# Performance work log

Measured on AMD Instinct MI355X. Metric: run time of the kernel, lower is better.

The kernel has to match this reference:

```python
import jax, jax.numpy as jnp
import numpy as np

N_USERS = 50000
N_ENTITIES = 100000
CHANNEL = 64
N_FACTORS = 4
N_REL = 9  # n_relations; weight has N_REL-1 rows
N_EDGES = 1_500_000
NNZ = 800_000
N_HOPS = 2


def _l2_normalize(x, eps=1e-12):
    # matches torch F.normalize(dim=1)
    n = jnp.sqrt(jnp.sum(x * x, axis=1, keepdims=True))
    return x / jnp.maximum(n, eps)


def _distance_correlation(t1, t2):
    # t1, t2: [d] rows of disen_weight_att (d = n_relations-1)
    ch = t1.shape[0]
    t1 = t1[:, None]
    t2 = t2[:, None]
    a_ = (t1 @ t1.T) * 2.0
    b_ = (t2 @ t2.T) * 2.0
    t1s = t1 ** 2
    t2s = t2 ** 2
    a = jnp.sqrt(jnp.maximum(t1s - a_ + t1s.T, 0.0) + 1e-8)
    b = jnp.sqrt(jnp.maximum(t2s - b_ + t2s.T, 0.0) + 1e-8)
    A = a - a.mean(axis=0, keepdims=True) - a.mean(axis=1, keepdims=True) + a.mean()
    B = b - b.mean(axis=0, keepdims=True) - b.mean(axis=1, keepdims=True) + b.mean()
    dcov_AB = jnp.sqrt(jnp.maximum((A * B).sum() / ch ** 2, 0.0) + 1e-8)
    dcov_AA = jnp.sqrt(jnp.maximum((A * A).sum() / ch ** 2, 0.0) + 1e-8)
    dcov_BB = jnp.sqrt(jnp.maximum((B * B).sum() / ch ** 2, 0.0) + 1e-8)
    return dcov_AB / jnp.sqrt(dcov_AA * dcov_BB + 1e-8)


def _cul_cor(disen_weight_att):
    cor = jnp.asarray(0.0, disen_weight_att.dtype)
    for i in range(N_FACTORS):
        for j in range(i + 1, N_FACTORS):
            cor = cor + _distance_correlation(disen_weight_att[i], disen_weight_att[j])
    return cor


def setup_inputs() -> dict:
    key = jax.random.key(0)
    ks = jax.random.split(key, 11)
    return {
        "user_emb": jax.random.normal(ks[0], (N_USERS, CHANNEL), jnp.float32) * 0.1,
        "entity_emb": jax.random.normal(ks[1], (N_ENTITIES, CHANNEL), jnp.float32) * 0.1,
        "latent_emb": jax.random.normal(ks[2], (N_FACTORS, CHANNEL), jnp.float32) * 0.1,
        "weight": jax.random.normal(ks[3], (N_REL - 1, CHANNEL), jnp.float32) * 0.1,
        "disen_weight_att": jax.random.normal(ks[4], (N_FACTORS, N_REL - 1), jnp.float32) * 0.1,
        "interact_vals": jax.random.uniform(ks[5], (NNZ,), jnp.float32),
        "head": jax.random.randint(ks[6], (N_EDGES,), 0, N_ENTITIES),
        "tail": jax.random.randint(ks[7], (N_EDGES,), 0, N_ENTITIES),
        "edge_type": jax.random.randint(ks[8], (N_EDGES,), 1, N_REL),  # in [1, N_REL-1]
        "interact_rows": jax.random.randint(ks[9], (NNZ,), 0, N_USERS),
        "interact_cols": jax.random.randint(ks[10], (NNZ,), 0, N_ENTITIES),
    }


def reference(user_emb, entity_emb, latent_emb, weight, disen_weight_att,
              interact_vals, head, tail, edge_type, interact_rows, interact_cols):
    n_entities = entity_emb.shape[0]
    n_users = user_emb.shape[0]
    cor = _cul_cor(disen_weight_att)

    entity_res = entity_emb
    user_res = user_emb
    ones_e = jnp.ones((head.shape[0],), entity_emb.dtype)
    cnt = jax.ops.segment_sum(ones_e, head, num_segments=n_entities)  # reused: head fixed
    cnt = jnp.maximum(cnt, 1.0)[:, None]

    for _ in range(N_HOPS):
        # KG aggregate: gather tail emb * relation emb, scatter-mean by head
        rel_emb = weight[edge_type - 1]                      # [E, C]
        msg = entity_emb[tail] * rel_emb                     # [E, C]
        entity_agg = jax.ops.segment_sum(msg, head, num_segments=n_entities) / cnt

        # user -> latent factor attention
        score = jax.nn.softmax(user_emb @ latent_emb.T, axis=1)   # [U, F]

        # user aggregate: sparse.mm(interact_mat, entity_emb)
        gathered = interact_vals[:, None] * entity_emb[interact_cols]  # [nnz, C]
        user_agg = jax.ops.segment_sum(gathered, interact_rows, num_segments=n_users)

        disen_weight = jax.nn.softmax(disen_weight_att, axis=-1) @ weight  # [F, C]
        mix = score @ disen_weight                                          # [U, C]
        user_new = user_agg * mix + user_agg

        entity_emb = _l2_normalize(entity_agg)
        user_emb = _l2_normalize(user_new)
        entity_res = entity_res + entity_emb
        user_res = user_res + user_emb

    return entity_res, user_res, cor
```

## Files before the change

### kernel.cpp

```cpp
#include <hip/hip_runtime.h>
#include <math.h>

constexpr int CH         = 64;
constexpr int N_USERS    = 50000;
constexpr int N_ENTITIES = 100000;
constexpr int N_FACTORS  = 4;
constexpr int N_RELM1    = 8;
constexpr int N_EDGES    = 1500000;
constexpr int NNZ        = 800000;

constexpr int NBE        = (N_ENTITIES + 255) / 256;
constexpr int NBU        = (N_USERS + 255) / 256;
constexpr int NBKT       = NBE + NBU;
constexpr int TOTAL      = N_EDGES + NNZ;
constexpr int IPB        = 4096;
constexpr int NBLK       = (TOTAL + IPB - 1) / IPB;
constexpr int CAP_E      = 4352;
constexpr int CAP_U      = 4608;
constexpr int ENT_BLK8   = N_ENTITIES / 8;
constexpr int USR_BLK8   = N_USERS / 8;

typedef unsigned int u32;
typedef float __attribute__((ext_vector_type(4))) f32x4;

__device__ __forceinline__ u32 pack_bf16x2(float a, float b) {
    u32 ua = __float_as_uint(a), ub = __float_as_uint(b);
    u32 ra = (ua + 0x7FFFu + ((ua >> 16) & 1u)) >> 16;
    u32 rb = (ub + 0x7FFFu + ((ub >> 16) & 1u)) >> 16;
    return ra | (rb << 16);
}
__device__ __forceinline__ float bf_lo(u32 v) { return __uint_as_float(v << 16); }
__device__ __forceinline__ float bf_hi(u32 v) { return __uint_as_float(v & 0xFFFF0000u); }

__device__ __forceinline__ float4 nt_ld4f(const float4* p) {
    f32x4 v = __builtin_nontemporal_load((const f32x4*)p);
    return make_float4(v.x, v.y, v.z, v.w);
}
__device__ __forceinline__ void nt_st4f(float4* p, float4 v) {
    f32x4 t; t.x = v.x; t.y = v.y; t.z = v.z; t.w = v.w;
    __builtin_nontemporal_store(t, (f32x4*)p);
}
__device__ __forceinline__ int   nt_ldi(const int* p)   { return __builtin_nontemporal_load(p); }
__device__ __forceinline__ float nt_ldf(const float* p) { return __builtin_nontemporal_load(p); }

__device__ __forceinline__ uint4 gz(const u32* __restrict__ t, int r, int c8, bool v) {
    uint4 x = make_uint4(0u, 0u, 0u, 0u);
    if (v) x = ((const uint4*)t)[r * 8 + c8];
    return x;
}


__global__ __launch_bounds__(256)
void fused_stage(const int* __restrict__ head, const int* __restrict__ tail,
                 const int* __restrict__ etype,
                 const int* __restrict__ irows, const int* __restrict__ icols,
                 const float* __restrict__ ivals,
                 int* __restrict__ Bcnt,
                 u32* __restrict__ stageE, u32* __restrict__ stageU,
                 float* __restrict__ stageUv) {
    __shared__ int hist[NBKT];
    __shared__ int cur[NBKT];
    for (int j = threadIdx.x; j < NBKT; j += 256) hist[j] = 0;
    __syncthreads();
    int start = blockIdx.x * IPB;
    int keys[IPB / 256];
    #pragma unroll
    for (int q = 0; q < IPB / 256; ++q) {
        int i = start + q * 256 + threadIdx.x;
        int k = 0;
        if (i < TOTAL) {
            if (i < N_EDGES) { k = head[i];            atomicAdd(&hist[k >> 8], 1); }
            else             { k = irows[i - N_EDGES]; atomicAdd(&hist[NBE + (k >> 8)], 1); }
        }
        keys[q] = k;
    }
    __syncthreads();
    for (int j = threadIdx.x; j < NBKT; j += 256) {
        int hv = hist[j];
        cur[j] = (hv > 0) ? atomicAdd(&Bcnt[j], hv) : 0;
    }
    __syncthreads();
    #pragma unroll
    for (int q = 0; q < IPB / 256; ++q) {
        int i = start + q * 256 + threadIdx.x;
        if (i >= TOTAL) continue;
        int k = keys[q];
        if (i < N_EDGES) {
            int b   = k >> 8;
            int rel = atomicAdd(&cur[b], 1);
            if (rel < CAP_E)
                stageE[b * CAP_E + rel] =
                    (u32)tail[i] | ((u32)(etype[i] - 1) << 17) | ((u32)(k & 255) << 20);
        } else {
            int ii  = i - N_EDGES;
            int b   = k >> 8;
            int rel = atomicAdd(&cur[NBE + b], 1);
            if (rel < CAP_U) {
                stageU[b * CAP_U + rel]  = (u32)icols[ii] | ((u32)(k & 255) << 17);
                stageUv[b * CAP_U + rel] = ivals[ii];
            }
        }
    }
}

__global__ __launch_bounds__(1024)
void scan587(const int* __restrict__ Bcnt, int* __restrict__ Bbase) {
    __shared__ int lds[1024];
    int t = threadIdx.x;
    int v = (t < NBE) ? min(Bcnt[t], CAP_E) : 0;
    lds[t] = v;
    __syncthreads();
    for (int d = 1; d < 1024; d <<= 1) {
        int u = (t >= d) ? lds[t - d] : 0;
        __syncthreads();
        lds[t] += u;
        __syncthreads();
    }
    if (t < NBE) Bbase[t] = lds[t] - v;
    __syncthreads();
    int v2 = (t < NBU) ? min(Bcnt[NBE + t], CAP_U) : 0;
    lds[t] = v2;
    __syncthreads();
    for (int d = 1; d < 1024; d <<= 1) {
        int u = (t >= d) ? lds[t - d] : 0;
        __syncthreads();
        lds[t] += u;
        __syncthreads();
    }
    if (t < NBU) Bbase[NBE + t] = lds[t] - v2;
}

__global__ __launch_bounds__(256)
void bin_fill2(const int* __restrict__ Bcnt, const int* __restrict__ Bbase,
               const u32* __restrict__ stageE, const u32* __restrict__ stageU,
               const float* __restrict__ stageUv,
               int* __restrict__ offE, int* __restrict__ offU,
               int* __restrict__ elst, int* __restrict__ ucol,
               float* __restrict__ uval) {
    __shared__ int khist[256];
    __shared__ int cur[256];
    __shared__ int wsum[4];
    int b = blockIdx.x, t = threadIdx.x;
    int w = t >> 6, lane = t & 63;
    khist[t] = 0;
    __syncthreads();
    if (b < NBE) {
        int n = min(Bcnt[b], CAP_E);
        const u32* src = stageE + b * CAP_E;
        for (int i = t; i < n; i += 256)
            atomicAdd(&khist[(src[i] >> 20) & 255], 1);
        __syncthreads();
        int v = khist[t];
        int incl = v;
        #pragma unroll
        for (int d = 1; d < 64; d <<= 1) {
            int u = __shfl_up(incl, d, 64);
            if (lane >= d) incl += u;
        }
        if (lane == 63) wsum[w] = incl;
        __syncthreads();
        int base = 0;
        #pragma unroll
        for (int q = 0; q < 4; ++q) if (q < w) base += wsum[q];
        int excl  = base + incl - v;
        int gbase = Bbase[b];
        int key   = b * 256 + t;
        if (key < N_ENTITIES) offE[key] = gbase + excl;
        cur[t] = gbase + excl;
        if (b == 0 && t == 0) offE[N_ENTITIES] = N_EDGES;
        __syncthreads();
        for (int i = t; i < n; i += 256) {
            u32 s = src[i];
            int p = atomicAdd(&cur[(s >> 20) & 255], 1);
            elst[p] = (int)(s & 0xFFFFFu);
        }
    } else {
        int bu = b - NBE;
        int n = min(Bcnt[b], CAP_U);
        const u32*   src  = stageU  + bu * CAP_U;
        const float* srcv = stageUv + bu * CAP_U;
        for (int i = t; i < n; i += 256)
            atomicAdd(&khist[(src[i] >> 17) & 255], 1);
        __syncthreads();
        int v = khist[t];
        int incl = v;
        #pragma unroll
        for (int d = 1; d < 64; d <<= 1) {
            int u = __shfl_up(incl, d, 64);
            if (lane >= d) incl += u;
        }
        if (lane == 63) wsum[w] = incl;
        __syncthreads();
        int base = 0;
        #pragma unroll
        for (int q = 0; q < 4; ++q) if (q < w) base += wsum[q];
        int excl  = base + incl - v;
        int gbase = Bbase[b];
        int key   = bu * 256 + t;
        if (key < N_USERS) offU[key] = gbase + excl;
        cur[t] = gbase + excl;
        if (b == NBE && t == 0) offU[N_USERS] = NNZ;
        __syncthreads();
        for (int i = t; i < n; i += 256) {
            u32 s = src[i];
            float vv = srcv[i];
            int p = atomicAdd(&cur[(s >> 17) & 255], 1);
            ucol[p] = (int)(s & 0x1FFFFu);
            uval[p] = vv;
        }
    }
}

__global__ __launch_bounds__(256)
void to_bf16(const float* __restrict__ src, u32* __restrict__ dst, int n2) {
    int i = blockIdx.x * 256 + threadIdx.x;
    if (i < n2) {
        float2 f = ((const float2*)src)[i];
        dst[i] = pack_bf16x2(f.x, f.y);
    }
}

__device__ __forceinline__ void acc_edge(float* acc, uint4 xv, float4 wa, float4 wb) {
    acc[0] += bf_lo(xv.x) * wa.x; acc[1] += bf_hi(xv.x) * wa.y;
    acc[2] += bf_lo(xv.y) * wa.z; acc[3] += bf_hi(xv.y) * wa.w;
    acc[4] += bf_lo(xv.z) * wb.x; acc[5] += bf_hi(xv.z) * wb.y;
    acc[6] += bf_lo(xv.w) * wb.z; acc[7] += bf_hi(xv.w) * wb.w;
}
__device__ __forceinline__ void acc_user(float* acc, uint4 xv, float vv) {
    acc[0] += vv * bf_lo(xv.x); acc[1] += vv * bf_hi(xv.x);
    acc[2] += vv * bf_lo(xv.y); acc[3] += vv * bf_hi(xv.y);
    acc[4] += vv * bf_lo(xv.z); acc[5] += vv * bf_hi(xv.z);
    acc[6] += vv * bf_lo(xv.w); acc[7] += vv * bf_hi(xv.w);
}

template <bool HOP0>
__global__ __launch_bounds__(256)
void hop_pass(const u32* __restrict__ entB,
              const float* __restrict__ usr_in,
              const float* __restrict__ weight, const float* __restrict__ latent,
              const float* __restrict__ dw,
              const int* __restrict__ offE, const int* __restrict__ elst,
              const int* __restrict__ offU, const int* __restrict__ ucol,
              const float* __restrict__ uval,
              u32* __restrict__ AeB_out,
              float* __restrict__ Au_out,
              float* __restrict__ ent_res, float* __restrict__ usr_res,
              const float* __restrict__ ent_base, const float* __restrict__ usr_base) {
    __shared__ float4 w4[N_RELM1 * 16];
    int lane = threadIdx.x & 63;
    int h    = lane >> 5;
    int g    = (lane >> 3) & 3;
    int c8   = lane & 7;
    int l5   = lane & 31;
    float acc[8] = {0.f, 0.f, 0.f, 0.f, 0.f, 0.f, 0.f, 0.f};

    if ((int)blockIdx.x < ENT_BLK8) {
        if (threadIdx.x < N_RELM1 * 16)
            w4[threadIdx.x] = ((const float4*)weight)[threadIdx.x];
        __syncthreads();
        int row = blockIdx.x * 8 + ((threadIdx.x >> 6) << 1) + h;
        int lo = offE[row], hi = offE[row + 1];
        for (int k0 = lo; k0 < hi; k0 += 32) {
            int m = min(32, hi - k0);
            int p = nt_ldi(&elst[min(k0 + l5, N_EDGES - 1)]);
            for (int jj = 0; jj < m; jj += 16) {
                int j0 = jj + g;
                int q0 = __shfl(p, j0,      32);
                int q1 = __shfl(p, j0 + 4,  32);
                int q2 = __shfl(p, j0 + 8,  32);
                int q3 = __shfl(p, j0 + 12, 32);
                uint4 x0 = gz(entB, q0 & 0x1FFFF, c8, j0      < m);
                uint4 x1 = gz(entB, q1 & 0x1FFFF, c8, j0 + 4  < m);
                uint4 x2 = gz(entB, q2 & 0x1FFFF, c8, j0 + 8  < m);
                uint4 x3 = gz(entB, q3 & 0x1FFFF, c8, j0 + 12 < m);
                float4 wa0 = w4[(q0 >> 17) * 16 + (c8 << 1)];
                float4 wb0 = w4[(q0 >> 17) * 16 + (c8 << 1) + 1];
                float4 wa1 = w4[(q1 >> 17) * 16 + (c8 << 1)];
                float4 wb1 = w4[(q1 >> 17) * 16 + (c8 << 1) + 1];
                float4 wa2 = w4[(q2 >> 17) * 16 + (c8 << 1)];
                float4 wb2 = w4[(q2 >> 17) * 16 + (c8 << 1) + 1];
                float4 wa3 = w4[(q3 >> 17) * 16 + (c8 << 1)];
                float4 wb3 = w4[(q3 >> 17) * 16 + (c8 << 1) + 1];
                acc_edge(acc, x0, wa0, wb0);
                acc_edge(acc, x1, wa1, wb1);
                acc_edge(acc, x2, wa2, wb2);
                acc_edge(acc, x3, wa3, wb3);
            }
        }
        #pragma unroll
        for (int j = 0; j < 8; ++j) {
            acc[j] += __shfl_xor(acc[j], 8, 64);
            acc[j] += __shfl_xor(acc[j], 16, 64);
        }
        float s = 0.0f;
        #pragma unroll
        for (int j = 0; j < 8; ++j) s += acc[j] * acc[j];
        s += __shfl_xor(s, 1, 64);
        s += __shfl_xor(s, 2, 64);
        s += __shfl_xor(s, 4, 64);
        float inv = 1.0f / fmaxf(sqrtf(s), 1e-12f);
        if (g == 0) {
            float y0 = acc[0] * inv, y1 = acc[1] * inv, y2 = acc[2] * inv, y3 = acc[3] * inv;
            float y4 = acc[4] * inv, y5 = acc[5] * inv, y6 = acc[6] * inv, y7 = acc[7] * inv;
            int qi = row * 16 + (c8 << 1);
            if (HOP0) {
                uint4 pk;
                pk.x = pack_bf16x2(y0, y1); pk.y = pack_bf16x2(y2, y3);
                pk.z = pack_bf16x2(y4, y5); pk.w = pack_bf16x2(y6, y7);
                ((uint4*)AeB_out)[row * 8 + c8] = pk;
                float4 b0 = nt_ld4f(&((const float4*)ent_base)[qi]);
                float4 b1 = nt_ld4f(&((const float4*)ent_base)[qi + 1]);
                nt_st4f(&((float4*)ent_res)[qi],     make_float4(b0.x + y0, b0.y + y1, b0.z + y2, b0.w + y3));
                nt_st4f(&((float4*)ent_res)[qi + 1], make_float4(b1.x + y4, b1.y + y5, b1.z + y6, b1.w + y7));
            } else {
                float4 r0 = nt_ld4f(&((const float4*)ent_res)[qi]);
                float4 r1 = nt_ld4f(&((const float4*)ent_res)[qi + 1]);
                nt_st4f(&((float4*)ent_res)[qi],     make_float4(r0.x + y0, r0.y + y1, r0.z + y2, r0.w + y3));
                nt_st4f(&((float4*)ent_res)[qi + 1], make_float4(r1.x + y4, r1.y + y5, r1.z + y6, r1.w + y7));
            }
        }
    } else {
        int row = (blockIdx.x - ENT_BLK8) * 8 + ((threadIdx.x >> 6) << 1) + h;
        int qi  = row * 16 + (c8 << 1);
        float4 u0 = nt_ld4f(&((const float4*)usr_in)[qi]);
        float4 u1 = nt_ld4f(&((const float4*)usr_in)[qi + 1]);
        int lo = offU[row], hi = offU[row + 1];
        for (int k0 = lo; k0 < hi; k0 += 32) {
            int m = min(32, hi - k0);
            int sidx = min(k0 + l5, NNZ - 1);
            int   cl = nt_ldi(&ucol[sidx]);
            float vl = nt_ldf(&uval[sidx]);
            for (int jj = 0; jj < m; jj += 16) {
                int j0 = jj + g;
                int   c0 = __shfl(cl, j0,      32);
                int   c1 = __shfl(cl, j0 + 4,  32);
                int   c2 = __shfl(cl, j0 + 8,  32);
                int   c3 = __shfl(cl, j0 + 12, 32);
                float v0 = __shfl(vl, j0,      32);
                float v1 = __shfl(vl, j0 + 4,  32);
                float v2 = __shfl(vl, j0 + 8,  32);
                float v3 = __shfl(vl, j0 + 12, 32);
                uint4 x0 = gz(entB, c0, c8, j0      < m);
                uint4 x1 = gz(entB, c1, c8, j0 + 4  < m);
                uint4 x2 = gz(entB, c2, c8, j0 + 8  < m);
                uint4 x3 = gz(entB, c3, c8, j0 + 12 < m);
                acc_user(acc, x0, v0);
                acc_user(acc, x1, v1);
                acc_user(acc, x2, v2);
                acc_user(acc, x3, v3);
            }
        }
        #pragma unroll
        for (int j = 0; j < 8; ++j) {
            acc[j] += __shfl_xor(acc[j], 8, 64);
            acc[j] += __shfl_xor(acc[j], 16, 64);
        }
        float d[N_FACTORS];
        #pragma unroll
        for (int f = 0; f < N_FACTORS; ++f) {
            float4 l0 = ((const float4*)latent)[f * 16 + (c8 << 1)];
            float4 l1 = ((const float4*)latent)[f * 16 + (c8 << 1) + 1];
            d[f] = u0.x * l0.x + u0.y * l0.y + u0.z * l0.z + u0.w * l0.w
                 + u1.x * l1.x + u1.y * l1.y + u1.z * l1.z + u1.w * l1.w;
            d[f] += __shfl_xor(d[f], 1, 64);
            d[f] += __shfl_xor(d[f], 2, 64);
            d[f] += __shfl_xor(d[f], 4, 64);
        }
        float mx = fmaxf(fmaxf(d[0], d[1]), fmaxf(d[2], d[3]));
        float ex0 = expf(d[0] - mx), ex1 = expf(d[1] - mx);
        float ex2 = expf(d[2] - mx), ex3 = expf(d[3] - mx);
        float sinv = 1.0f / (ex0 + ex1 + ex2 + ex3);
        float mix[8] = {0.f, 0.f, 0.f, 0.f, 0.f, 0.f, 0.f, 0.f};
        {
            float exf[N_FACTORS] = {ex0, ex1, ex2, ex3};
            #pragma unroll
            for (int f = 0; f < N_FACTORS; ++f) {
                float4 w0 = ((const float4*)dw)[f * 16 + (c8 << 1)];
                float4 w1 = ((const float4*)dw)[f * 16 + (c8 << 1) + 1];
                float ef = exf[f];
                mix[0] += ef * w0.x; mix[1] += ef * w0.y;
                mix[2] += ef * w0.z; mix[3] += ef * w0.w;
                mix[4] += ef * w1.x; mix[5] += ef * w1.y;
                mix[6] += ef * w1.z; mix[7] += ef * w1.w;
            }
            #pragma unroll
            for (int j = 0; j < 8; ++j) mix[j] *= sinv;
        }
        float un[8];
        #pragma unroll
        for (int j = 0; j < 8; ++j) un[j] = acc[j] * (1.0f + mix[j]);
        float s = 0.0f;
        #pragma unroll
        for (int j = 0; j < 8; ++j) s += un[j] * un[j];
        s += __shfl_xor(s, 1, 64);
        s += __shfl_xor(s, 2, 64);
        s += __shfl_xor(s, 4, 64);
        float inv = 1.0f / fmaxf(sqrtf(s), 1e-12f);
        if (g == 0) {
            float y0 = un[0] * inv, y1 = un[1] * inv, y2 = un[2] * inv, y3 = un[3] * inv;
            float y4 = un[4] * inv, y5 = un[5] * inv, y6 = un[6] * inv, y7 = un[7] * inv;
            if (HOP0) {
                nt_st4f(&((float4*)Au_out)[qi],     make_float4(y0, y1, y2, y3));
                nt_st4f(&((float4*)Au_out)[qi + 1], make_float4(y4, y5, y6, y7));
            } else {
                float4 b0 = nt_ld4f(&((const float4*)usr_base)[qi]);
                float4 b1 = nt_ld4f(&((const float4*)usr_base)[qi + 1]);
                nt_st4f(&((float4*)usr_res)[qi],
                        make_float4((b0.x + u0.x) + y0, (b0.y + u0.y) + y1,
                                    (b0.z + u0.z) + y2, (b0.w + u0.w) + y3));
                nt_st4f(&((float4*)usr_res)[qi + 1],
                        make_float4((b1.x + u1.x) + y4, (b1.y + u1.y) + y5,
                                    (b1.z + u1.z) + y6, (b1.w + u1.w) + y7));
            }
        }
    }
}

__global__ __launch_bounds__(384)
void discor_kernel(const float* __restrict__ att,
                   const float* __restrict__ weight,
                   float* __restrict__ dw,
                   float* __restrict__ cor_out) {
    __shared__ float part[6];
    if (blockIdx.x == 0) {
        if (threadIdx.x < 256) {
            int f = threadIdx.x >> 6;
            int c = threadIdx.x & 63;
            float m = -1e30f;
            #pragma unroll
            for (int j = 0; j < N_RELM1; ++j) m = fmaxf(m, att[f * N_RELM1 + j]);
            float s = 0.0f, w[N_RELM1];
            #pragma unroll
            for (int j = 0; j < N_RELM1; ++j) { w[j] = expf(att[f * N_RELM1 + j] - m); s += w[j]; }
            float acc = 0.0f;
            #pragma unroll
            for (int j = 0; j < N_RELM1; ++j) acc += w[j] * weight[j * CH + c];
            dw[f * CH + c] = acc / s;
        }
    } else {
        int w    = threadIdx.x >> 6;
        int lane = threadIdx.x & 63;
        const int pi[6] = {0, 0, 0, 1, 1, 2};
        const int pj[6] = {1, 2, 3, 2, 3, 3};
        int r = lane >> 3, c = lane & 7;
        const float* t1 = att + pi[w] * N_RELM1;
        const float* t2 = att + pj[w] * N_RELM1;
        float a  = sqrtf(fmaxf(t1[r] * t1[r] - 2.0f * t1[r] * t1[c] + t1[c] * t1[c], 0.0f) + 1e-8f);
        float bb = sqrtf(fmaxf(t2[r] * t2[r] - 2.0f * t2[r] * t2[c] + t2[c] * t2[c], 0.0f) + 1e-8f);
        float rsA = a, rsB = bb;
        #pragma unroll
        for (int o = 1; o < 8; o <<= 1) { rsA += __shfl_xor(rsA, o, 64); rsB += __shfl_xor(rsB, o, 64); }
        float csA = a, csB = bb;
        #pragma unroll
        for (int o = 8; o < 64; o <<= 1) { csA += __shfl_xor(csA, o, 64); csB += __shfl_xor(csB, o, 64); }
        float totA = rsA, totB = rsB;
        #pragma unroll
        for (int o = 8; o < 64; o <<= 1) { totA += __shfl_xor(totA, o, 64); totB += __shfl_xor(totB, o, 64); }
        float A = a  - csA * 0.125f - rsA * 0.125f + totA * (1.0f / 64.0f);
        float B = bb - csB * 0.125f - rsB * 0.125f + totB * (1.0f / 64.0f);
        float sAB = A * B, sAA = A * A, sBB = B * B;
        #pragma unroll
        for (int o = 1; o < 64; o <<= 1) {
            sAB += __shfl_xor(sAB, o, 64);
            sAA += __shfl_xor(sAA, o, 64);
            sBB += __shfl_xor(sBB, o, 64);
        }
        if (lane == 0) {
            float dAB = sqrtf(fmaxf(sAB * (1.0f / 64.0f), 0.0f) + 1e-8f);
            float dAA = sqrtf(fmaxf(sAA * (1.0f / 64.0f), 0.0f) + 1e-8f);
            float dBB = sqrtf(fmaxf(sBB * (1.0f / 64.0f), 0.0f) + 1e-8f);
            part[w] = dAB / sqrtf(dAA * dBB + 1e-8f);
        }
        __syncthreads();
        if (threadIdx.x == 0) {
            float s = 0.0f;
            for (int q = 0; q < 6; ++q) s += part[q];
            cor_out[0] = s;
        }
    }
}

extern "C" void kernel_launch(void* const* d_in, const int* in_sizes, int n_in,
                              void* d_out, int out_size, void* d_ws, size_t ws_size,
                              hipStream_t stream) {
    const float* user_emb   = (const float*)d_in[0];
    const float* entity_emb = (const float*)d_in[1];
    const float* latent     = (const float*)d_in[2];
    const float* weight     = (const float*)d_in[3];
    const float* att        = (const float*)d_in[4];
    const float* ivals      = (const float*)d_in[5];
    const int*   head       = (const int*)d_in[6];
    const int*   tail       = (const int*)d_in[7];
    const int*   etype      = (const int*)d_in[8];
    const int*   irows      = (const int*)d_in[9];
    const int*   icols      = (const int*)d_in[10];

    float* out     = (float*)d_out;
    float* ent_res = out;
    float* usr_res = out + (size_t)N_ENTITIES * CH;
    float* cor_out = out + (size_t)N_ENTITIES * CH + (size_t)N_USERS * CH;

    const size_t ENT_ELEMS = (size_t)N_ENTITIES * CH;
    const size_t USR_ELEMS = (size_t)N_USERS * CH;
    const int    ENT_PAIRS = (int)(ENT_ELEMS / 2);

    float* ws   = (float*)d_ws;
    u32*   entB = (u32*)ws;
    u32*   AeB  = entB + ENT_PAIRS;
    float* Au   = (float*)(AeB + ENT_PAIRS);
    float* dw   = Au + USR_ELEMS;
    int*   offE = (int*)(dw + N_FACTORS * CH);
    int*   offU = offE + N_ENTITIES + 1;
    int*   elst = offU + N_USERS + 1;
    int*   ucol = elst + N_EDGES;
    float* uval = (float*)(ucol + NNZ);
    int*   Bcnt  = (int*)Au;
    int*   Bbase = Bcnt + NBKT;
    u32*   stageE  = entB;
    u32*   stageU  = stageE + (size_t)NBE * CAP_E;
    float* stageUv = (float*)(stageU + (size_t)NBU * CAP_U);

    discor_kernel<<<2, 384, 0, stream>>>(att, weight, dw, cor_out);

    hipMemsetAsync(Bcnt, 0, (size_t)NBKT * sizeof(int), stream);
    fused_stage<<<NBLK, 256, 0, stream>>>(head, tail, etype, irows, icols, ivals,
                                          Bcnt, stageE, stageU, stageUv);
    scan587<<<1, 1024, 0, stream>>>(Bcnt, Bbase);
    bin_fill2<<<NBKT, 256, 0, stream>>>(Bcnt, Bbase, stageE, stageU, stageUv,
                                        offE, offU, elst, ucol, uval);

    to_bf16<<<(ENT_PAIRS + 255) / 256, 256, 0, stream>>>(entity_emb, entB, ENT_PAIRS);

    hop_pass<true><<<ENT_BLK8 + USR_BLK8, 256, 0, stream>>>(
        entB, user_emb, weight, latent, dw,
        offE, elst, offU, ucol, uval,
        AeB, Au, ent_res, usr_res, entity_emb, user_emb);

    hop_pass<false><<<ENT_BLK8 + USR_BLK8, 256, 0, stream>>>(
        AeB, Au, weight, latent, dw,
        offE, elst, offU, ucol, uval,
        nullptr, nullptr, ent_res, usr_res, entity_emb, user_emb);
}
```

Before: 337.9 us.

## Merge staging, bf16 conversion and discor into one kernel; fold scan into bin fill

Combines the bucket staging pass, the entity bf16 conversion and the disentangle/correlation work into a single launch using block-index ranges. The separate 587-bucket scan kernel is removed, and each bin_fill block computes its own base by summing the preceding bucket counts. Staging buffers move to the AeB region so they no longer alias entB, and the nontemporal loads of edge lists are replaced with plain loads. This cuts three launches and their serialization, at the cost of redundant prefix summation in every bin_fill block.

```diff
diff --git a/kernel.cpp b/kernel.cpp
--- a/kernel.cpp
+++ b/kernel.cpp
@@ -17,6 +17,9 @@
 constexpr int NBLK       = (TOTAL + IPB - 1) / IPB;
 constexpr int CAP_E      = 4352;
 constexpr int CAP_U      = 4608;
+constexpr int ENT_PAIRS_ = (N_ENTITIES * CH) / 2;
+constexpr int NBF16B     = ENT_PAIRS_ / 256;
+constexpr int MEGA_BLKS  = NBLK + NBF16B + 2;
 constexpr int ENT_BLK8   = N_ENTITIES / 8;
 constexpr int USR_BLK8   = N_USERS / 8;
 
@@ -40,8 +43,6 @@
     f32x4 t; t.x = v.x; t.y = v.y; t.z = v.z; t.w = v.w;
     __builtin_nontemporal_store(t, (f32x4*)p);
 }
-__device__ __forceinline__ int   nt_ldi(const int* p)   { return __builtin_nontemporal_load(p); }
-__device__ __forceinline__ float nt_ldf(const float* p) { return __builtin_nontemporal_load(p); }
 
 __device__ __forceinline__ uint4 gz(const u32* __restrict__ t, int r, int c8, bool v) {
     uint4 x = make_uint4(0u, 0u, 0u, 0u);
@@ -49,89 +50,127 @@
     return x;
 }
 
-
 __global__ __launch_bounds__(256)
-void fused_stage(const int* __restrict__ head, const int* __restrict__ tail,
-                 const int* __restrict__ etype,
-                 const int* __restrict__ irows, const int* __restrict__ icols,
-                 const float* __restrict__ ivals,
-                 int* __restrict__ Bcnt,
-                 u32* __restrict__ stageE, u32* __restrict__ stageU,
-                 float* __restrict__ stageUv) {
+void mega_stage(const int* __restrict__ head, const int* __restrict__ tail,
+                const int* __restrict__ etype,
+                const int* __restrict__ irows, const int* __restrict__ icols,
+                const float* __restrict__ ivals,
+                int* __restrict__ Bcnt,
+                u32* __restrict__ stageE, u32* __restrict__ stageU,
+                float* __restrict__ stageUv,
+                const float* __restrict__ entity_emb, u32* __restrict__ entB,
+                const float* __restrict__ att, const float* __restrict__ weight,
+                float* __restrict__ dw, float* __restrict__ cor_out) {
     __shared__ int hist[NBKT];
     __shared__ int cur[NBKT];
-    for (int j = threadIdx.x; j < NBKT; j += 256) hist[j] = 0;
-    __syncthreads();
-    int start = blockIdx.x * IPB;
-    int keys[IPB / 256];
-    #pragma unroll
-    for (int q = 0; q < IPB / 256; ++q) {
-        int i = start + q * 256 + threadIdx.x;
-        int k = 0;
-        if (i < TOTAL) {
-            if (i < N_EDGES) { k = head[i];            atomicAdd(&hist[k >> 8], 1); }
-            else             { k = irows[i - N_EDGES]; atomicAdd(&hist[NBE + (k >> 8)], 1); }
-        }
-        keys[q] = k;
+    __shared__ float part[6];
+    int bid = blockIdx.x;
+    if (bid < NBLK) {
+        for (int j = threadIdx.x; j < NBKT; j += 256) hist[j] = 0;
+        __syncthreads();
+        int start = bid * IPB;
+        int keys[IPB / 256];
+        #pragma unroll
+        for (int q = 0; q < IPB / 256; ++q) {
+            int i = start + q * 256 + threadIdx.x;
+            int k = 0;
+            if (i < TOTAL) {
+                if (i < N_EDGES) { k = head[i];            atomicAdd(&hist[k >> 8], 1); }
+                else             { k = irows[i - N_EDGES]; atomicAdd(&hist[NBE + (k >> 8)], 1); }
+            }
+            keys[q] = k;
+        }
+        __syncthreads();
+        for (int j = threadIdx.x; j < NBKT; j += 256) {
+            int hv = hist[j];
+            cur[j] = (hv > 0) ? atomicAdd(&Bcnt[j], hv) : 0;
+        }
+        __syncthreads();
+        #pragma unroll
+        for (int q = 0; q < IPB / 256; ++q) {
+            int i = start + q * 256 + threadIdx.x;
+            if (i >= TOTAL) continue;
+            int k = keys[q];
+            if (i < N_EDGES) {
+                int b   = k >> 8;
+                int rel = atomicAdd(&cur[b], 1);
+                if (rel < CAP_E)
+                    stageE[b * CAP_E + rel] =
+                        (u32)tail[i] | ((u32)(etype[i] - 1) << 17) | ((u32)(k & 255) << 20);
+            } else {
+                int ii  = i - N_EDGES;
+                int b   = k >> 8;
+                int rel = atomicAdd(&cur[NBE + b], 1);
+                if (rel < CAP_U) {
+                    stageU[b * CAP_U + rel]  = (u32)icols[ii] | ((u32)(k & 255) << 17);
+                    stageUv[b * CAP_U + rel] = ivals[ii];
+                }
+            }
+        }
+    } else if (bid < NBLK + NBF16B) {
+        int i = (bid - NBLK) * 256 + threadIdx.x;
+        float2 f = ((const float2*)entity_emb)[i];
+        entB[i] = pack_bf16x2(f.x, f.y);
+    } else if (bid == NBLK + NBF16B) {
+        int f = threadIdx.x >> 6;
+        int c = threadIdx.x & 63;
+        float m = -1e30f;
+        #pragma unroll
+        for (int j = 0; j < N_RELM1; ++j) m = fmaxf(m, att[f * N_RELM1 + j]);
+        float s = 0.0f, w[N_RELM1];
+        #pragma unroll
+        for (int j = 0; j < N_RELM1; ++j) { w[j] = expf(att[f * N_RELM1 + j] - m); s += w[j]; }
+        float acc = 0.0f;
+        #pragma unroll
+        for (int j = 0; j < N_RELM1; ++j) acc += w[j] * weight[j * CH + c];
+        dw[f * CH + c] = acc / s;
+    } else {
+        int w    = threadIdx.x >> 6;
+        int lane = threadIdx.x & 63;
+        const int pi[6] = {0, 0, 0, 1, 1, 2};
+        const int pj[6] = {1, 2, 3, 2, 3, 3};
+        int r = lane >> 3, c = lane & 7;
+        for (int pp = w; pp < 6; pp += 4) {
+            const float* t1 = att + pi[pp] * N_RELM1;
+            const float* t2 = att + pj[pp] * N_RELM1;
+            float a  = sqrtf(fmaxf(t1[r] * t1[r] - 2.0f * t1[r] * t1[c] + t1[c] * t1[c], 0.0f) + 1e-8f);
+            float bb = sqrtf(fmaxf(t2[r] * t2[r] - 2.0f * t2[r] * t2[c] + t2[c] * t2[c], 0.0f) + 1e-8f);
+            float rsA = a, rsB = bb;
+            #pragma unroll
+            for (int o = 1; o < 8; o <<= 1) { rsA += __shfl_xor(rsA, o, 64); rsB += __shfl_xor(rsB, o, 64); }
+            float csA = a, csB = bb;
+            #pragma unroll
+            for (int o = 8; o < 64; o <<= 1) { csA += __shfl_xor(csA, o, 64); csB += __shfl_xor(csB, o, 64); }
+            float totA = rsA, totB = rsB;
+            #pragma unroll
+            for (int o = 8; o < 64; o <<= 1) { totA += __shfl_xor(totA, o, 64); totB += __shfl_xor(totB, o, 64); }
+            float A = a  - csA * 0.125f - rsA * 0.125f + totA * (1.0f / 64.0f);
+            float B = bb - csB * 0.125f - rsB * 0.125f + totB * (1.0f / 64.0f);
+            float sAB = A * B, sAA = A * A, sBB = B * B;
+            #pragma unroll
+            for (int o = 1; o < 64; o <<= 1) {
+                sAB += __shfl_xor(sAB, o, 64);
+                sAA += __shfl_xor(sAA, o, 64);
+                sBB += __shfl_xor(sBB, o, 64);
+            }
+            if (lane == 0) {
+                float dAB = sqrtf(fmaxf(sAB * (1.0f / 64.0f), 0.0f) + 1e-8f);
+                float dAA = sqrtf(fmaxf(sAA * (1.0f / 64.0f), 0.0f) + 1e-8f);
+                float dBB = sqrtf(fmaxf(sBB * (1.0f / 64.0f), 0.0f) + 1e-8f);
+                part[pp] = dAB / sqrtf(dAA * dBB + 1e-8f);
+            }
+        }
+        __syncthreads();
+        if (threadIdx.x == 0) {
+            float s = 0.0f;
+            for (int q = 0; q < 6; ++q) s += part[q];
+            cor_out[0] = s;
+        }
     }
-    __syncthreads();
-    for (int j = threadIdx.x; j < NBKT; j += 256) {
-        int hv = hist[j];
-        cur[j] = (hv > 0) ? atomicAdd(&Bcnt[j], hv) : 0;
-    }
-    __syncthreads();
-    #pragma unroll
-    for (int q = 0; q < IPB / 256; ++q) {
-        int i = start + q * 256 + threadIdx.x;
-        if (i >= TOTAL) continue;
-        int k = keys[q];
-        if (i < N_EDGES) {
-            int b   = k >> 8;
-            int rel = atomicAdd(&cur[b], 1);
-            if (rel < CAP_E)
-                stageE[b * CAP_E + rel] =
-                    (u32)tail[i] | ((u32)(etype[i] - 1) << 17) | ((u32)(k & 255) << 20);
-        } else {
-            int ii  = i - N_EDGES;
-            int b   = k >> 8;
-            int rel = atomicAdd(&cur[NBE + b], 1);
-            if (rel < CAP_U) {
-                stageU[b * CAP_U + rel]  = (u32)icols[ii] | ((u32)(k & 255) << 17);
-                stageUv[b * CAP_U + rel] = ivals[ii];
-            }
-        }
-    }
-}
-
-__global__ __launch_bounds__(1024)
-void scan587(const int* __restrict__ Bcnt, int* __restrict__ Bbase) {
-    __shared__ int lds[1024];
-    int t = threadIdx.x;
-    int v = (t < NBE) ? min(Bcnt[t], CAP_E) : 0;
-    lds[t] = v;
-    __syncthreads();
-    for (int d = 1; d < 1024; d <<= 1) {
-        int u = (t >= d) ? lds[t - d] : 0;
-        __syncthreads();
-        lds[t] += u;
-        __syncthreads();
-    }
-    if (t < NBE) Bbase[t] = lds[t] - v;
-    __syncthreads();
-    int v2 = (t < NBU) ? min(Bcnt[NBE + t], CAP_U) : 0;
-    lds[t] = v2;
-    __syncthreads();
-    for (int d = 1; d < 1024; d <<= 1) {
-        int u = (t >= d) ? lds[t - d] : 0;
-        __syncthreads();
-        lds[t] += u;
-        __syncthreads();
-    }
-    if (t < NBU) Bbase[NBE + t] = lds[t] - v2;
 }
 
 __global__ __launch_bounds__(256)
-void bin_fill2(const int* __restrict__ Bcnt, const int* __restrict__ Bbase,
+void bin_fill3(const int* __restrict__ Bcnt,
                const u32* __restrict__ stageE, const u32* __restrict__ stageU,
                const float* __restrict__ stageUv,
                int* __restrict__ offE, int* __restrict__ offU,
@@ -142,9 +181,20 @@
     __shared__ int wsum[4];
     int b = blockIdx.x, t = threadIdx.x;
     int w = t >> 6, lane = t & 63;
+    bool isE = (b < NBE);
+    int seg0 = isE ? 0 : NBE;
+    int cap  = isE ? CAP_E : CAP_U;
+    int partial = 0;
+    for (int i = seg0 + t; i < b; i += 256) partial += min(Bcnt[i], cap);
+    #pragma unroll
+    for (int o = 1; o < 64; o <<= 1) partial += __shfl_xor(partial, o, 64);
+    if (lane == 0) wsum[w] = partial;
+    __syncthreads();
+    int gbase = wsum[0] + wsum[1] + wsum[2] + wsum[3];
+    __syncthreads();
     khist[t] = 0;
     __syncthreads();
-    if (b < NBE) {
+    if (isE) {
         int n = min(Bcnt[b], CAP_E);
         const u32* src = stageE + b * CAP_E;
         for (int i = t; i < n; i += 256)
@@ -162,9 +212,8 @@
         int base = 0;
         #pragma unroll
         for (int q = 0; q < 4; ++q) if (q < w) base += wsum[q];
-        int excl  = base + incl - v;
-        int gbase = Bbase[b];
-        int key   = b * 256 + t;
+        int excl = base + incl - v;
+        int key  = b * 256 + t;
         if (key < N_ENTITIES) offE[key] = gbase + excl;
         cur[t] = gbase + excl;
         if (b == 0 && t == 0) offE[N_ENTITIES] = N_EDGES;
@@ -194,9 +243,8 @@
         int base = 0;
         #pragma unroll
         for (int q = 0; q < 4; ++q) if (q < w) base += wsum[q];
-        int excl  = base + incl - v;
-        int gbase = Bbase[b];
-        int key   = bu * 256 + t;
+        int excl = base + incl - v;
+        int key  = bu * 256 + t;
         if (key < N_USERS) offU[key] = gbase + excl;
         cur[t] = gbase + excl;
         if (b == NBE && t == 0) offU[N_USERS] = NNZ;
@@ -208,15 +256,6 @@
             ucol[p] = (int)(s & 0x1FFFFu);
             uval[p] = vv;
         }
-    }
-}
-
-__global__ __launch_bounds__(256)
-void to_bf16(const float* __restrict__ src, u32* __restrict__ dst, int n2) {
-    int i = blockIdx.x * 256 + threadIdx.x;
-    if (i < n2) {
-        float2 f = ((const float2*)src)[i];
-        dst[i] = pack_bf16x2(f.x, f.y);
     }
 }
 
@@ -262,7 +301,7 @@
         int lo = offE[row], hi = offE[row + 1];
         for (int k0 = lo; k0 < hi; k0 += 32) {
             int m = min(32, hi - k0);
-            int p = nt_ldi(&elst[min(k0 + l5, N_EDGES - 1)]);
+            int p = elst[min(k0 + l5, N_EDGES - 1)];
             for (int jj = 0; jj < m; jj += 16) {
                 int j0 = jj + g;
                 int q0 = __shfl(p, j0,      32);
@@ -328,8 +367,8 @@
         for (int k0 = lo; k0 < hi; k0 += 32) {
             int m = min(32, hi - k0);
             int sidx = min(k0 + l5, NNZ - 1);
-            int   cl = nt_ldi(&ucol[sidx]);
-            float vl = nt_ldf(&uval[sidx]);
+            int   cl = ucol[sidx];
+            float vl = uval[sidx];
             for (int jj = 0; jj < m; jj += 16) {
                 int j0 = jj + g;
                 int   c0 = __shfl(cl, j0,      32);
@@ -416,70 +455,6 @@
     }
 }
 
-__global__ __launch_bounds__(384)
-void discor_kernel(const float* __restrict__ att,
-                   const float* __restrict__ weight,
-                   float* __restrict__ dw,
-                   float* __restrict__ cor_out) {
-    __shared__ float part[6];
-    if (blockIdx.x == 0) {
-        if (threadIdx.x < 256) {
-            int f = threadIdx.x >> 6;
-            int c = threadIdx.x & 63;
-            float m = -1e30f;
-            #pragma unroll
-            for (int j = 0; j < N_RELM1; ++j) m = fmaxf(m, att[f * N_RELM1 + j]);
-            float s = 0.0f, w[N_RELM1];
-            #pragma unroll
-            for (int j = 0; j < N_RELM1; ++j) { w[j] = expf(att[f * N_RELM1 + j] - m); s += w[j]; }
-            float acc = 0.0f;
-            #pragma unroll
-            for (int j = 0; j < N_RELM1; ++j) acc += w[j] * weight[j * CH + c];
-            dw[f * CH + c] = acc / s;
-        }
-    } else {
-        int w    = threadIdx.x >> 6;
-        int lane = threadIdx.x & 63;
-        const int pi[6] = {0, 0, 0, 1, 1, 2};
-        const int pj[6] = {1, 2, 3, 2, 3, 3};
-        int r = lane >> 3, c = lane & 7;
-        const float* t1 = att + pi[w] * N_RELM1;
-        const float* t2 = att + pj[w] * N_RELM1;
-        float a  = sqrtf(fmaxf(t1[r] * t1[r] - 2.0f * t1[r] * t1[c] + t1[c] * t1[c], 0.0f) + 1e-8f);
-        float bb = sqrtf(fmaxf(t2[r] * t2[r] - 2.0f * t2[r] * t2[c] + t2[c] * t2[c], 0.0f) + 1e-8f);
-        float rsA = a, rsB = bb;
-        #pragma unroll
-        for (int o = 1; o < 8; o <<= 1) { rsA += __shfl_xor(rsA, o, 64); rsB += __shfl_xor(rsB, o, 64); }
-        float csA = a, csB = bb;
-        #pragma unroll
-        for (int o = 8; o < 64; o <<= 1) { csA += __shfl_xor(csA, o, 64); csB += __shfl_xor(csB, o, 64); }
-        float totA = rsA, totB = rsB;
-        #pragma unroll
-        for (int o = 8; o < 64; o <<= 1) { totA += __shfl_xor(totA, o, 64); totB += __shfl_xor(totB, o, 64); }
-        float A = a  - csA * 0.125f - rsA * 0.125f + totA * (1.0f / 64.0f);
-        float B = bb - csB * 0.125f - rsB * 0.125f + totB * (1.0f / 64.0f);
-        float sAB = A * B, sAA = A * A, sBB = B * B;
-        #pragma unroll
-        for (int o = 1; o < 64; o <<= 1) {
-            sAB += __shfl_xor(sAB, o, 64);
-            sAA += __shfl_xor(sAA, o, 64);
-            sBB += __shfl_xor(sBB, o, 64);
-        }
-        if (lane == 0) {
-            float dAB = sqrtf(fmaxf(sAB * (1.0f / 64.0f), 0.0f) + 1e-8f);
-            float dAA = sqrtf(fmaxf(sAA * (1.0f / 64.0f), 0.0f) + 1e-8f);
-            float dBB = sqrtf(fmaxf(sBB * (1.0f / 64.0f), 0.0f) + 1e-8f);
-            part[w] = dAB / sqrtf(dAA * dBB + 1e-8f);
-        }
-        __syncthreads();
-        if (threadIdx.x == 0) {
-            float s = 0.0f;
-            for (int q = 0; q < 6; ++q) s += part[q];
-            cor_out[0] = s;
-        }
-    }
-}
-
 extern "C" void kernel_launch(void* const* d_in, const int* in_sizes, int n_in,
                               void* d_out, int out_size, void* d_ws, size_t ws_size,
                               hipStream_t stream) {
@@ -514,22 +489,18 @@
     int*   elst = offU + N_USERS + 1;
     int*   ucol = elst + N_EDGES;
     float* uval = (float*)(ucol + NNZ);
-    int*   Bcnt  = (int*)Au;
-    int*   Bbase = Bcnt + NBKT;
-    u32*   stageE  = entB;
+    u32*   stageE  = AeB;
     u32*   stageU  = stageE + (size_t)NBE * CAP_E;
     float* stageUv = (float*)(stageU + (size_t)NBU * CAP_U);
-
-    discor_kernel<<<2, 384, 0, stream>>>(att, weight, dw, cor_out);
+    int*   Bcnt = (int*)(Au + 1000000);
 
     hipMemsetAsync(Bcnt, 0, (size_t)NBKT * sizeof(int), stream);
-    fused_stage<<<NBLK, 256, 0, stream>>>(head, tail, etype, irows, icols, ivals,
-                                          Bcnt, stageE, stageU, stageUv);
-    scan587<<<1, 1024, 0, stream>>>(Bcnt, Bbase);
-    bin_fill2<<<NBKT, 256, 0, stream>>>(Bcnt, Bbase, stageE, stageU, stageUv,
+    mega_stage<<<MEGA_BLKS, 256, 0, stream>>>(head, tail, etype, irows, icols, ivals,
+                                              Bcnt, stageE, stageU, stageUv,
+                                              entity_emb, entB,
+                                              att, weight, dw, cor_out);
+    bin_fill3<<<NBKT, 256, 0, stream>>>(Bcnt, stageE, stageU, stageUv,
                                         offE, offU, elst, ucol, uval);
-
-    to_bf16<<<(ENT_PAIRS + 255) / 256, 256, 0, stream>>>(entity_emb, entB, ENT_PAIRS);
 
     hop_pass<true><<<ENT_BLK8 + USR_BLK8, 256, 0, stream>>>(
         entB, user_emb, weight, latent, dw,
```

Measured after the change: 333.6 us. Within noise of the previous version (-1.3%).
